# Kernel tuning notes

Measured on AMD Instinct MI355X. Metric: run time of the kernel, lower is better.

## Reference

```python
import math
import jax, jax.numpy as jnp
import numpy as np

B = 16; ENC_S = 64; ENC_T = 96
SCALE = 64; POOL = 16; DM = 256; NH = 16
E_LAYERS = 3; D_LAYERS = 2; DFF = 1024
OUT_S = 64; OUT_T = 32
LN_EPS = 1e-5


def _pe(d_model, length):
    pos = np.arange(length, dtype=np.float32)[:, None]
    div = np.exp(np.arange(0, d_model, 2, dtype=np.float32) * (-math.log(10000.0) / d_model))
    pe = np.zeros((length, d_model), np.float32)
    pe[:, 0::2] = np.sin(pos * div)
    pe[:, 1::2] = np.cos(pos * div)
    return jnp.asarray(pe)


def _conv1d_circ(x, w, b):
    # x: (N, C, L), w: (O, C, 3); torch Conv1d(padding=1, padding_mode='circular')
    xp = jnp.pad(x, ((0, 0), (0, 0), (1, 1)), mode='wrap')
    y = jax.lax.conv_general_dilated(xp, w, (1,), 'VALID',
                                     dimension_numbers=('NCH', 'OIH', 'NCH'))
    return y + b[None, :, None]


def _layernorm(x, w, b):
    mu = jnp.mean(x, -1, keepdims=True)
    var = jnp.var(x, -1, keepdims=True)
    return (x - mu) * jax.lax.rsqrt(var + LN_EPS) * w + b


def _data_embedding(x, sproj_w, sproj_b, scproj_w, scproj_b, tok_w, tok_b):
    Bb = x.shape[0]
    h = _conv1d_circ(jnp.swapaxes(x, 1, 2), sproj_w, sproj_b)       # (B, enc_t, enc_t)
    h = _conv1d_circ(h, scproj_w, scproj_b)                          # (B, scale, enc_t)
    h = _conv1d_circ(jnp.swapaxes(h, 1, 2), scproj_w, scproj_b)     # (B, scale, scale)
    h = h.reshape(Bb * SCALE, 1, SCALE)
    tok = jnp.swapaxes(_conv1d_circ(h, tok_w, tok_b), 1, 2)          # (B*scale, scale, dm)
    emb = tok + _pe(DM, SCALE)[None]
    return emb.reshape(Bb, SCALE, SCALE, DM)


def _lin_attn(q, k, v, causal):
    # q,k,v: (Bp, L, H, E); k/v adaptively avg-pooled over L to POOL (L % POOL == 0)
    Bp, L, H, E = q.shape
    win = L // POOL
    kp = k.reshape(Bp, POOL, win, H, E).mean(axis=2)
    vp = v.reshape(Bp, POOL, win, H, E).mean(axis=2)
    scores = jnp.einsum('blhe,bshe->bhls', q, kp)      # (Bp, H, L, POOL)
    if causal:
        m = jnp.arange(POOL)[None, :] > jnp.arange(L)[:, None]
        scores = jnp.where(m[None, None], -jnp.inf, scores)
    A = jax.nn.softmax(scores / math.sqrt(E), axis=-1)
    return jnp.einsum('bhls,bshd->blhd', A, vp)


def _st_attn(x, kv, Wq, bq, Wo, bo, causal):
    Bb, T, S, dm = x.shape
    H = NH // 2
    proj = lambda z: z @ Wq.T + bq
    # faithful to source: query_projection used for q, k AND v; views are flat reshapes
    qt = proj(x.reshape(Bb * S, T, dm)).reshape(Bb * S, T, H, -1)
    qs = proj(x.reshape(Bb * T, S, dm)).reshape(Bb * T, S, H, -1)
    kt = proj(kv.reshape(Bb * S, T, dm)).reshape(Bb * S, T, H, -1)
    ks = proj(kv.reshape(Bb * T, S, dm)).reshape(Bb * T, S, H, -1)
    out_t = _lin_attn(qt, kt, kt, causal).reshape(Bb, S, T, -1)
    out_s = _lin_attn(qs, ks, ks, causal).reshape(Bb, S, T, -1)
    out = jnp.concatenate([out_t, out_s], axis=-1).reshape(Bb, S * T, 2 * dm)
    out = out @ Wo.T + bo
    return out.reshape(Bb, T, S, dm)


def _ffn(x, c1w, c1b, c2w, c2b):
    # conv1d kernel_size=1 over the T axis of (B*S, T, dm) == pointwise GEMM
    Bb, T, S, dm = x.shape
    y = x.reshape(Bb * S, T, dm)
    y = jax.nn.gelu(jnp.einsum('ntd,fd->ntf', y, c1w) + c1b, approximate=False)
    y = jnp.einsum('ntf,df->ntd', y, c2w) + c2b
    return y.reshape(Bb, T, S, dm)


def _forward(x_enc, x_dec,
             enc_sproj_w, enc_sproj_b, enc_scproj_w, enc_scproj_b, enc_tok_w, enc_tok_b,
             dec_sproj_w, dec_sproj_b, dec_scproj_w, dec_scproj_b, dec_tok_w, dec_tok_b,
             e_Wq, e_bq, e_Wo, e_bo, e_c1w, e_c1b, e_c2w, e_c2b,
             e_ln1w, e_ln1b, e_ln2w, e_ln2b, enc_norm_w, enc_norm_b,
             d_sWq, d_sbq, d_sWo, d_sbo, d_cWq, d_cbq, d_cWo, d_cbo,
             d_c1w, d_c1b, d_c2w, d_c2b,
             d_ln1w, d_ln1b, d_ln2w, d_ln2b, d_ln3w, d_ln3b,
             dec_norm_w, dec_norm_b, proj_w, proj_b):
    enc = _data_embedding(x_enc, enc_sproj_w, enc_sproj_b, enc_scproj_w, enc_scproj_b, enc_tok_w, enc_tok_b)
    for i in range(E_LAYERS):
        h = enc + _st_attn(enc, enc, e_Wq[i], e_bq[i], e_Wo[i], e_bo[i], False)
        h = _layernorm(h, e_ln1w[i], e_ln1b[i])
        enc = _layernorm(h + _ffn(h, e_c1w[i], e_c1b[i], e_c2w[i], e_c2b[i]), e_ln2w[i], e_ln2b[i])
    enc = _layernorm(enc, enc_norm_w, enc_norm_b)
    dec = _data_embedding(x_dec, dec_sproj_w, dec_sproj_b, dec_scproj_w, dec_scproj_b, dec_tok_w, dec_tok_b)
    for i in range(D_LAYERS):
        h = dec + _st_attn(dec, dec, d_sWq[i], d_sbq[i], d_sWo[i], d_sbo[i], True)
        h = _layernorm(h, d_ln1w[i], d_ln1b[i])
        h = h + _st_attn(h, enc, d_cWq[i], d_cbq[i], d_cWo[i], d_cbo[i], False)
        h = _layernorm(h, d_ln2w[i], d_ln2b[i])
        dec = _layernorm(h + _ffn(h, d_c1w[i], d_c1b[i], d_c2w[i], d_c2b[i]), d_ln3w[i], d_ln3b[i])
    dec = _layernorm(dec, dec_norm_w, dec_norm_b)
    dec = dec.mean(axis=2)                 # (B, scale, dm)
    out = dec @ proj_w.T + proj_b          # (B, scale, out_s)
    return out[:, -OUT_T:, :]


def setup_inputs() -> dict:
    keys = iter(jax.random.split(jax.random.key(0), 80))
    def nrm(shape, s=0.02):
        return jax.random.normal(next(keys), shape, jnp.float32) * s
    E, D = E_LAYERS, D_LAYERS
    inp = {
        'x_enc': nrm((B, ENC_T, ENC_S), 1.0),
        'x_dec': nrm((B, ENC_T, ENC_S), 1.0),
    }
    for p in ('enc', 'dec'):
        inp[p + '_sproj_w'] = nrm((ENC_T, ENC_S, 3)); inp[p + '_sproj_b'] = nrm((ENC_T,))
        inp[p + '_scproj_w'] = nrm((SCALE, ENC_T, 3)); inp[p + '_scproj_b'] = nrm((SCALE,))
        inp[p + '_tok_w'] = nrm((DM, 1, 3), 0.1); inp[p + '_tok_b'] = nrm((DM,))
    inp.update(
        e_Wq=nrm((E, DM, DM)), e_bq=nrm((E, DM)),
        e_Wo=nrm((E, DM, 2 * DM)), e_bo=nrm((E, DM)),
        e_c1w=nrm((E, DFF, DM)), e_c1b=nrm((E, DFF)),
        e_c2w=nrm((E, DM, DFF)), e_c2b=nrm((E, DM)),
        e_ln1w=jnp.ones((E, DM)), e_ln1b=jnp.zeros((E, DM)),
        e_ln2w=jnp.ones((E, DM)), e_ln2b=jnp.zeros((E, DM)),
        enc_norm_w=jnp.ones((DM,)), enc_norm_b=jnp.zeros((DM,)),
        d_sWq=nrm((D, DM, DM)), d_sbq=nrm((D, DM)),
        d_sWo=nrm((D, DM, 2 * DM)), d_sbo=nrm((D, DM)),
        d_cWq=nrm((D, DM, DM)), d_cbq=nrm((D, DM)),
        d_cWo=nrm((D, DM, 2 * DM)), d_cbo=nrm((D, DM)),
        d_c1w=nrm((D, DFF, DM)), d_c1b=nrm((D, DFF)),
        d_c2w=nrm((D, DM, DFF)), d_c2b=nrm((D, DM)),
        d_ln1w=jnp.ones((D, DM)), d_ln1b=jnp.zeros((D, DM)),
        d_ln2w=jnp.ones((D, DM)), d_ln2b=jnp.zeros((D, DM)),
        d_ln3w=jnp.ones((D, DM)), d_ln3b=jnp.zeros((D, DM)),
        dec_norm_w=jnp.ones((DM,)), dec_norm_b=jnp.zeros((DM,)),
        proj_w=nrm((OUT_S, DM)), proj_b=nrm((OUT_S,)),
    )
    return inp


def reference(x_enc, x_dec,
              enc_sproj_w, enc_sproj_b, enc_scproj_w, enc_scproj_b, enc_tok_w, enc_tok_b,
              dec_sproj_w, dec_sproj_b, dec_scproj_w, dec_scproj_b, dec_tok_w, dec_tok_b,
              e_Wq, e_bq, e_Wo, e_bo, e_c1w, e_c1b, e_c2w, e_c2b,
              e_ln1w, e_ln1b, e_ln2w, e_ln2b, enc_norm_w, enc_norm_b,
              d_sWq, d_sbq, d_sWo, d_sbo, d_cWq, d_cbq, d_cWo, d_cbo,
              d_c1w, d_c1b, d_c2w, d_c2b,
              d_ln1w, d_ln1b, d_ln2w, d_ln2b, d_ln3w, d_ln3b,
              dec_norm_w, dec_norm_b, proj_w, proj_b):
    return _forward(x_enc, x_dec,
                    enc_sproj_w, enc_sproj_b, enc_scproj_w, enc_scproj_b, enc_tok_w, enc_tok_b,
                    dec_sproj_w, dec_sproj_b, dec_scproj_w, dec_scproj_b, dec_tok_w, dec_tok_b,
                    e_Wq, e_bq, e_Wo, e_bo, e_c1w, e_c1b, e_c2w, e_c2b,
                    e_ln1w, e_ln1b, e_ln2w, e_ln2b, enc_norm_w, enc_norm_b,
                    d_sWq, d_sbq, d_sWo, d_sbo, d_cWq, d_cbq, d_cWo, d_cbo,
                    d_c1w, d_c1b, d_c2w, d_c2b,
                    d_ln1w, d_ln1b, d_ln2w, d_ln2b, d_ln3w, d_ln3b,
                    dec_norm_w, dec_norm_b, proj_w, proj_b)
```

## Files before the change

### kernel.cpp

```cpp
#include <hip/hip_runtime.h>


typedef unsigned short u16;
typedef short s16;
typedef __attribute__((ext_vector_type(8))) s16 bfrag;
typedef __attribute__((ext_vector_type(4))) float f32x4;

__device__ __forceinline__ float b2f(u16 u) {
  union { float f; unsigned int i; } v; v.i = ((unsigned int)u) << 16; return v.f;
}
__device__ __forceinline__ u16 f2b(float f) {
  union { float f; unsigned int i; } v; v.f = f;
  unsigned int x = v.i;
  return (u16)((x + 0x7FFFu + ((x >> 16) & 1u)) >> 16);
}
__device__ __forceinline__ float gelu_f(float v) {
  float u = 0.7978845608f * v * (1.0f + 0.044715f * v * v);
  float e = __expf(2.0f * u);
  return v * (1.0f - 1.0f / (e + 1.0f));
}

__device__ __forceinline__ void gload16(const void* g, void* l) {
  __builtin_amdgcn_global_load_lds(
      (const __attribute__((address_space(1))) unsigned int*)g,
      (__attribute__((address_space(3))) unsigned int*)l, 16, 0, 0);
}

__global__ void ws_signal(float* out, float v) { out[0] = v; }

__global__ void cvt_bf(const float* __restrict__ src, u16* __restrict__ dst, int n) {
  int i = blockIdx.x * 256 + threadIdx.x;
  if (i < n) dst[i] = f2b(src[i]);
}
__global__ void weff_bf(const float* __restrict__ Wo, u16* __restrict__ W) {
  int n = blockIdx.x, k = threadIdx.x;
  W[n * 256 + k] = f2b(Wo[n * 512 + k] + Wo[n * 512 + 256 + k]);
}

__global__ void pe_kernel(float* __restrict__ pe) {
  int l = blockIdx.x, d = threadIdx.x;
  int i = d >> 1;
  float div = expf((float)(2 * i) * (-9.210340371976184f / 256.0f));
  float ang = (float)l * div;
  pe[l * 256 + d] = (d & 1) ? cosf(ang) : sinf(ang);
}

__global__ void conv_sproj(const float* __restrict__ x, const float* __restrict__ w,
                           const float* __restrict__ bias, float* __restrict__ h1) {
  int o = blockIdx.x, b = blockIdx.y, l = threadIdx.x;
  const float* wo = w + o * 192;
  const float* xb = x + (size_t)b * 96 * 64;
  float acc = bias[o];
#pragma unroll
  for (int k = 0; k < 3; ++k) {
    int lp = l + k - 1; if (lp < 0) lp += 96; if (lp >= 96) lp -= 96;
    const float* xr = xb + lp * 64;
    for (int c = 0; c < 64; ++c) acc = fmaf(xr[c], wo[c * 3 + k], acc);
  }
  h1[((size_t)b * 96 + o) * 96 + l] = acc;
}

__global__ void conv_scproj_t(const float* __restrict__ h1, const float* __restrict__ w,
                              const float* __restrict__ bias, float* __restrict__ h2) {
  int o = blockIdx.x, b = blockIdx.y, l = threadIdx.x;
  const float* wo = w + o * 288;
  const float* hb = h1 + (size_t)b * 96 * 96;
  float acc = bias[o];
#pragma unroll
  for (int k = 0; k < 3; ++k) {
    int lp = l + k - 1; if (lp < 0) lp += 96; if (lp >= 96) lp -= 96;
    for (int c = 0; c < 96; ++c) acc = fmaf(hb[c * 96 + lp], wo[c * 3 + k], acc);
  }
  h2[((size_t)b * 64 + o) * 96 + l] = acc;
}

__global__ void conv_scproj_s(const float* __restrict__ h2, const float* __restrict__ w,
                              const float* __restrict__ bias, float* __restrict__ h3) {
  int o = blockIdx.x, b = blockIdx.y, l = threadIdx.x;
  const float* wo = w + o * 288;
  const float* hb = h2 + (size_t)b * 64 * 96;
  float acc = bias[o];
#pragma unroll
  for (int k = 0; k < 3; ++k) {
    int lp = l + k - 1; if (lp < 0) lp += 64; if (lp >= 64) lp -= 64;
    for (int c = 0; c < 96; ++c) acc = fmaf(hb[lp * 96 + c], wo[c * 3 + k], acc);
  }
  h3[((size_t)b * 64 + o) * 64 + l] = acc;
}

__global__ void tok_embed(const float* __restrict__ h3, const float* __restrict__ w,
                          const float* __restrict__ bias, const float* __restrict__ pe,
                          u16* __restrict__ E) {
  int g = blockIdx.x, d = threadIdx.x;
  __shared__ float row[64];
  if (d < 64) row[d] = h3[(size_t)g * 64 + d];
  __syncthreads();
  float w0 = w[d * 3], w1 = w[d * 3 + 1], w2 = w[d * 3 + 2], bd = bias[d];
  for (int j = 0; j < 64; ++j) {
    int jm = (j + 63) & 63, jp = (j + 1) & 63;
    float v = bd + row[jm] * w0 + row[j] * w1 + row[jp] * w2 + pe[j * 256 + d];
    E[((size_t)g * 64 + j) * 256 + d] = f2b(v);
  }
}

template <int ACT, int NBX>
__global__ __launch_bounds__(256) void mfma_gemm(const u16* __restrict__ A,
                                                 const u16* __restrict__ W,
                                                 const float* __restrict__ bias,
                                                 u16* __restrict__ C, int N, int K,
                                                 int nby) {
  __shared__ s16 smem[8192];
  s16* As = smem;
  s16* Bs = smem + 4096;
  constexpr int LB = (NBX == 8) ? 3 : 1;
  int f = blockIdx.x;
  int q = (NBX * nby) >> 3;
  int w = (f & 7) * q + (f >> 3);
  int bx = w & (NBX - 1), by = w >> LB;
  int t = threadIdx.x;
  int wave = t >> 6, lane = t & 63;
  int wr = wave >> 1, wc = wave & 1;
  int row0 = by * 128, col0 = bx * 128;
  int kc = (lane >> 4) & 3, rr = lane & 15;
  const u16* Ap0 = A + (size_t)(row0 + wave * 16 + rr) * K + kc * 8;
  const u16* Ap1 = A + (size_t)(row0 + (wave + 4) * 16 + rr) * K + kc * 8;
  const u16* Bp0 = W + (size_t)(col0 + wave * 16 + rr) * K + kc * 8;
  const u16* Bp1 = W + (size_t)(col0 + (wave + 4) * 16 + rr) * K + kc * 8;
  s16* lA0 = As + wave * 512;
  s16* lA1 = As + (wave + 4) * 512;
  s16* lB0 = Bs + wave * 512;
  s16* lB1 = Bs + (wave + 4) * 512;
  f32x4 acc[4][4];
#pragma unroll
  for (int m = 0; m < 4; ++m)
#pragma unroll
    for (int n = 0; n < 4; ++n) acc[m][n] = (f32x4){0.f, 0.f, 0.f, 0.f};
  for (int k0 = 0; k0 < K; k0 += 32) {
    gload16(Ap0 + k0, lA0);
    gload16(Ap1 + k0, lA1);
    gload16(Bp0 + k0, lB0);
    gload16(Bp1 + k0, lB1);
    __syncthreads();
    bfrag af[4], bf[4];
#pragma unroll
    for (int m = 0; m < 4; ++m) af[m] = *(const bfrag*)(As + ((wr * 4 + m) * 64 + lane) * 8);
#pragma unroll
    for (int n = 0; n < 4; ++n) bf[n] = *(const bfrag*)(Bs + ((wc * 4 + n) * 64 + lane) * 8);
#pragma unroll
    for (int m = 0; m < 4; ++m)
#pragma unroll
      for (int n = 0; n < 4; ++n)
        acc[m][n] = __builtin_amdgcn_mfma_f32_16x16x32_bf16(af[m], bf[n], acc[m][n], 0, 0, 0);
    __syncthreads();
  }
  s16* Cs = smem;
  int g4 = (lane >> 4) << 2;
  int cl = lane & 15;
  float bc[4];
#pragma unroll
  for (int n = 0; n < 4; ++n) bc[n] = bias[col0 + wc * 64 + n * 16 + cl];
#pragma unroll
  for (int P = 0; P < 4; ++P) {
    __syncthreads();
    if (wr == (P >> 1)) {
#pragma unroll
      for (int mm = 0; mm < 2; ++mm) {
        int m = (P & 1) * 2 + mm;
#pragma unroll
        for (int n = 0; n < 4; ++n) {
#pragma unroll
          for (int r = 0; r < 4; ++r) {
            float v = acc[m][n][r] + bc[n];
            if (ACT == 1) v = gelu_f(v);
            Cs[(mm * 16 + g4 + r) * 136 + wc * 64 + n * 16 + cl] = (s16)f2b(v);
          }
        }
      }
    }
    __syncthreads();
#pragma unroll
    for (int it = 0; it < 2; ++it) {
      int idx = it * 256 + t;
      int lr = idx >> 4, slot = idx & 15;
      *(uint4*)(C + (size_t)(row0 + P * 32 + lr) * N + col0 + slot * 8) =
          *(const uint4*)(Cs + lr * 136 + slot * 8);
    }
  }
}

__global__ __launch_bounds__(512) void mfma_gemm_resln(const u16* __restrict__ X,
                                                       const u16* __restrict__ W,
                                                       const float* __restrict__ bias,
                                                       u16* __restrict__ R,
                                                       const float* __restrict__ lnw,
                                                       const float* __restrict__ lnb,
                                                       int K) {
  __shared__ s16 smem[12288];
  __shared__ float pls[32][4][2];
  s16* As = smem;
  s16* Bs = smem + 4096;
  int t = threadIdx.x;
  int wave = t >> 6, lane = t & 63;
  int wr = wave >> 2, wc = wave & 3;
  int row0 = blockIdx.x * 128;
  int kc = (lane >> 4) & 3, rr = lane & 15;
  const u16* Xp = X + (size_t)(row0 + wave * 16 + rr) * K + kc * 8;
  const u16* Wp0 = W + (size_t)(wave * 16 + rr) * K + kc * 8;
  const u16* Wp1 = W + (size_t)((wave + 8) * 16 + rr) * K + kc * 8;
  s16* lA = As + wave * 512;
  s16* lB0 = Bs + wave * 512;
  s16* lB1 = Bs + (wave + 8) * 512;
  f32x4 acc[4][4];
#pragma unroll
  for (int m = 0; m < 4; ++m)
#pragma unroll
    for (int n = 0; n < 4; ++n) acc[m][n] = (f32x4){0.f, 0.f, 0.f, 0.f};
  for (int k0 = 0; k0 < K; k0 += 32) {
    gload16(Xp + k0, lA);
    gload16(Wp0 + k0, lB0);
    gload16(Wp1 + k0, lB1);
    __syncthreads();
    bfrag af[4], bf[4];
#pragma unroll
    for (int m = 0; m < 4; ++m) af[m] = *(const bfrag*)(As + ((wr * 4 + m) * 64 + lane) * 8);
#pragma unroll
    for (int n = 0; n < 4; ++n) bf[n] = *(const bfrag*)(Bs + ((wc * 4 + n) * 64 + lane) * 8);
#pragma unroll
    for (int m = 0; m < 4; ++m)
#pragma unroll
      for (int n = 0; n < 4; ++n)
        acc[m][n] = __builtin_amdgcn_mfma_f32_16x16x32_bf16(af[m], bf[n], acc[m][n], 0, 0, 0);
    __syncthreads();
  }
  s16* Rs = smem;
  int g4 = (lane >> 4) << 2;
  int cl = lane & 15;
  float lw[4], lb[4], bc[4];
#pragma unroll
  for (int n = 0; n < 4; ++n) {
    int col = wc * 64 + n * 16 + cl;
    bc[n] = bias[col]; lw[n] = lnw[col]; lb[n] = lnb[col];
  }
#pragma unroll
  for (int P = 0; P < 4; ++P) {
    bool own = (wr == (P >> 1));
    __syncthreads();
#pragma unroll
    for (int it = 0; it < 2; ++it) {
      int idx = it * 512 + t;
      int lr = idx >> 5, slot = idx & 31;
      *(uint4*)(Rs + lr * 264 + slot * 8) =
          *(const uint4*)(R + (size_t)(row0 + P * 32 + lr) * 256 + slot * 8);
    }
    __syncthreads();
    if (own) {
#pragma unroll
      for (int mm = 0; mm < 2; ++mm) {
        int m = (P & 1) * 2 + mm;
#pragma unroll
        for (int r = 0; r < 4; ++r) {
          int lr = mm * 16 + g4 + r;
          float s = 0.f, s2 = 0.f;
#pragma unroll
          for (int n = 0; n < 4; ++n) {
            float v = acc[m][n][r] + bc[n] +
                      b2f((u16)Rs[lr * 264 + wc * 64 + n * 16 + cl]);
            acc[m][n][r] = v;
            s += v; s2 = fmaf(v, v, s2);
          }
#pragma unroll
          for (int o = 1; o < 16; o <<= 1) { s += __shfl_xor(s, o); s2 += __shfl_xor(s2, o); }
          if (cl == 0) { pls[lr][wc][0] = s; pls[lr][wc][1] = s2; }
        }
      }
    }
    __syncthreads();
    if (own) {
#pragma unroll
      for (int mm = 0; mm < 2; ++mm) {
        int m = (P & 1) * 2 + mm;
#pragma unroll
        for (int r = 0; r < 4; ++r) {
          int lr = mm * 16 + g4 + r;
          float s = pls[lr][0][0] + pls[lr][1][0] + pls[lr][2][0] + pls[lr][3][0];
          float s2 = pls[lr][0][1] + pls[lr][1][1] + pls[lr][2][1] + pls[lr][3][1];
          float mu = s * (1.0f / 256.0f);
          float var = fmaxf(s2 * (1.0f / 256.0f) - mu * mu, 0.0f);
          float rs = rsqrtf(var + 1e-5f);
#pragma unroll
          for (int n = 0; n < 4; ++n) {
            Rs[lr * 264 + wc * 64 + n * 16 + cl] =
                (s16)f2b((acc[m][n][r] - mu) * rs * lw[n] + lb[n]);
          }
        }
      }
    }
    __syncthreads();
#pragma unroll
    for (int it = 0; it < 2; ++it) {
      int idx = it * 512 + t;
      int lr = idx >> 5, slot = idx & 31;
      *(uint4*)(R + (size_t)(row0 + P * 32 + lr) * 256 + slot * 8) =
          *(const uint4*)(Rs + lr * 264 + slot * 8);
    }
  }
}

template <int CROSS, int CAUSAL>
__global__ __launch_bounds__(512) void lin_attn(u16* __restrict__ Q,
                                                const u16* __restrict__ KP) {
  __shared__ u16 qs[64 * 264];
  __shared__ float kpool[16][260];
  int p = blockIdx.x, t = threadIdx.x;
  u16* Qg = Q + (size_t)p * 16384;
#pragma unroll
  for (int i = 0; i < 4; ++i) {
    int idx = i * 512 + t;
    int row = idx >> 5, slot = idx & 31;
    *(uint4*)(qs + row * 264 + slot * 8) = *(const uint4*)(Qg + row * 256 + slot * 8);
  }
  __syncthreads();
  if (CROSS) {
    for (int idx = t; idx < 4096; idx += 512) {
      int s = idx >> 8, d = idx & 255;
      kpool[s][d] = b2f(KP[((size_t)p * 16 + s) * 256 + d]);
    }
  } else {
    for (int idx = t; idx < 4096; idx += 512) {
      int s = idx >> 8, d = idx & 255;
      const u16* b0 = qs + (4 * s) * 264 + d;
      kpool[s][d] = 0.25f * (b2f(b0[0]) + b2f(b0[264]) + b2f(b0[528]) + b2f(b0[792]));
    }
  }
  __syncthreads();
  int h = t >> 6, l = t & 63;
  u16* q = qs + l * 264 + h * 32;
  float qr[32];
#pragma unroll
  for (int e = 0; e < 32; e += 4) {
    ushort4 v = *(const ushort4*)&q[e];
    qr[e] = b2f(v.x); qr[e + 1] = b2f(v.y); qr[e + 2] = b2f(v.z); qr[e + 3] = b2f(v.w);
  }
  float sc[16], mx = -INFINITY;
#pragma unroll
  for (int s = 0; s < 16; ++s) {
    const float* kp = &kpool[s][h * 32];
    float d = 0.f;
#pragma unroll
    for (int e = 0; e < 32; ++e) d = fmaf(qr[e], kp[e], d);
    d *= 0.17677669529663687f;
    if (CAUSAL && s > l) d = -INFINITY;
    sc[s] = d; mx = fmaxf(mx, d);
  }
  float sum = 0.f;
#pragma unroll
  for (int s = 0; s < 16; ++s) { sc[s] = expf(sc[s] - mx); sum += sc[s]; }
  float inv = 1.0f / sum;
  float o[32] = {};
#pragma unroll
  for (int s = 0; s < 16; ++s) {
    float a = sc[s] * inv;
    const float* vp = &kpool[s][h * 32];
#pragma unroll
    for (int e = 0; e < 32; ++e) o[e] = fmaf(a, vp[e], o[e]);
  }
#pragma unroll
  for (int e = 0; e < 32; e += 4) {
    ushort4 v;
    v.x = f2b(o[e]); v.y = f2b(o[e + 1]); v.z = f2b(o[e + 2]); v.w = f2b(o[e + 3]);
    *(ushort4*)&q[e] = v;
  }
  __syncthreads();
#pragma unroll
  for (int i = 0; i < 4; ++i) {
    int idx = i * 512 + t;
    int row = idx >> 5, slot = idx & 31;
    *(uint4*)(Qg + row * 256 + slot * 8) = *(const uint4*)(qs + row * 264 + slot * 8);
  }
}

__global__ __launch_bounds__(256) void ln_bf(u16* __restrict__ X,
                                             const float* __restrict__ w,
                                             const float* __restrict__ b) {
  int lane = threadIdx.x & 63, wv = threadIdx.x >> 6;
  size_t row = (size_t)blockIdx.x * 4 + wv;
  size_t off = row * 256 + lane * 4;
  ushort4 xv = *(const ushort4*)(X + off);
  float v0 = b2f(xv.x), v1 = b2f(xv.y), v2 = b2f(xv.z), v3 = b2f(xv.w);
  float s = v0 + v1 + v2 + v3;
  float s2 = v0 * v0 + v1 * v1 + v2 * v2 + v3 * v3;
#pragma unroll
  for (int o = 32; o; o >>= 1) { s += __shfl_xor(s, o); s2 += __shfl_xor(s2, o); }
  float mu = s * (1.0f / 256.0f);
  float var = fmaxf(s2 * (1.0f / 256.0f) - mu * mu, 0.0f);
  float rs = rsqrtf(var + 1e-5f);
  float4 w4 = *(const float4*)(w + lane * 4);
  float4 b4 = *(const float4*)(b + lane * 4);
  ushort4 o4;
  o4.x = f2b((v0 - mu) * rs * w4.x + b4.x);
  o4.y = f2b((v1 - mu) * rs * w4.y + b4.y);
  o4.z = f2b((v2 - mu) * rs * w4.z + b4.z);
  o4.w = f2b((v3 - mu) * rs * w4.w + b4.w);
  *(ushort4*)(X + off) = o4;
}

__global__ void pool_bf(const u16* __restrict__ A, u16* __restrict__ P) {
  int r = blockIdx.x, d = threadIdx.x;
  int g = r >> 4, s = r & 15;
  const u16* src = A + ((size_t)g * 64 + 4 * (size_t)s) * 256 + d;
  float v = 0.25f * (b2f(src[0]) + b2f(src[256]) + b2f(src[512]) + b2f(src[768]));
  P[(size_t)r * 256 + d] = f2b(v);
}

__global__ __launch_bounds__(256) void mean_proj_bf(const u16* __restrict__ X,
                                                    const float* __restrict__ pw,
                                                    const float* __restrict__ pb,
                                                    float* __restrict__ out) {
  int bid = blockIdx.x;
  int b = bid >> 5, ii = bid & 31;
  int i = 32 + ii;
  __shared__ float md[256];
  int d = threadIdx.x;
  const u16* base = X + ((size_t)b * 64 + i) * 64 * 256 + d;
  float s = 0.f;
  for (int j = 0; j < 64; ++j) s += b2f(base[(size_t)j * 256]);
  md[d] = s * (1.0f / 64.0f);
  __syncthreads();
  if (d < 64) {
    float acc = pb[d];
    const float* wr = pw + d * 256;
    for (int k = 0; k < 256; ++k) acc = fmaf(md[k], wr[k], acc);
    out[((size_t)b * 32 + ii) * 64 + d] = acc;
  }
}

extern "C" void kernel_launch(void* const* d_in, const int* in_sizes, int n_in,
                              void* d_out, int out_size, void* d_ws, size_t ws_size,
                              hipStream_t stream) {
  (void)in_sizes; (void)out_size;
  if (n_in < 50) return;

  const float* x_enc = (const float*)d_in[0];
  const float* x_dec = (const float*)d_in[1];
  const float* enc_sproj_w = (const float*)d_in[2];
  const float* enc_sproj_b = (const float*)d_in[3];
  const float* enc_scproj_w = (const float*)d_in[4];
  const float* enc_scproj_b = (const float*)d_in[5];
  const float* enc_tok_w = (const float*)d_in[6];
  const float* enc_tok_b = (const float*)d_in[7];
  const float* dec_sproj_w = (const float*)d_in[8];
  const float* dec_sproj_b = (const float*)d_in[9];
  const float* dec_scproj_w = (const float*)d_in[10];
  const float* dec_scproj_b = (const float*)d_in[11];
  const float* dec_tok_w = (const float*)d_in[12];
  const float* dec_tok_b = (const float*)d_in[13];
  const float* e_Wq = (const float*)d_in[14];
  const float* e_bq = (const float*)d_in[15];
  const float* e_Wo = (const float*)d_in[16];
  const float* e_bo = (const float*)d_in[17];
  const float* e_c1w = (const float*)d_in[18];
  const float* e_c1b = (const float*)d_in[19];
  const float* e_c2w = (const float*)d_in[20];
  const float* e_c2b = (const float*)d_in[21];
  const float* e_ln1w = (const float*)d_in[22];
  const float* e_ln1b = (const float*)d_in[23];
  const float* e_ln2w = (const float*)d_in[24];
  const float* e_ln2b = (const float*)d_in[25];
  const float* enc_norm_w = (const float*)d_in[26];
  const float* enc_norm_b = (const float*)d_in[27];
  const float* d_sWq = (const float*)d_in[28];
  const float* d_sbq = (const float*)d_in[29];
  const float* d_sWo = (const float*)d_in[30];
  const float* d_sbo = (const float*)d_in[31];
  const float* d_cWq = (const float*)d_in[32];
  const float* d_cbq = (const float*)d_in[33];
  const float* d_cWo = (const float*)d_in[34];
  const float* d_cbo = (const float*)d_in[35];
  const float* d_c1w = (const float*)d_in[36];
  const float* d_c1b = (const float*)d_in[37];
  const float* d_c2w = (const float*)d_in[38];
  const float* d_c2b = (const float*)d_in[39];
  const float* d_ln1w = (const float*)d_in[40];
  const float* d_ln1b = (const float*)d_in[41];
  const float* d_ln2w = (const float*)d_in[42];
  const float* d_ln2b = (const float*)d_in[43];
  const float* d_ln3w = (const float*)d_in[44];
  const float* d_ln3b = (const float*)d_in[45];
  const float* dec_norm_w = (const float*)d_in[46];
  const float* dec_norm_b = (const float*)d_in[47];
  const float* proj_w = (const float*)d_in[48];
  const float* proj_b = (const float*)d_in[49];

  const size_t ACT = 16777216;
  const size_t POOLE = 4194304;
  const size_t WBN = 3538944;
  size_t base_need = (3 * ACT + 2 * POOLE + WBN) * 2 +
                     (size_t)(16384 + 147456 + 98304 + 65536) * 4;
  if (ws_size < base_need) {
    ws_signal<<<1, 1, 0, stream>>>((float*)d_out, (float)(ws_size >> 20));
    return;
  }
  char* wsb = (char*)d_ws;
  u16* A_enc = (u16*)wsb;  wsb += ACT * 2;
  u16* A_dec = (u16*)wsb;  wsb += ACT * 2;
  u16* T1 = (u16*)wsb;     wsb += ACT * 2;
  u16* PA = (u16*)wsb;     wsb += POOLE * 2;
  u16* PK = (u16*)wsb;     wsb += POOLE * 2;
  u16* WB = (u16*)wsb;     wsb += WBN * 2;
  float* PE = (float*)wsb;  wsb += 16384 * 4;
  float* EH1 = (float*)wsb; wsb += 147456 * 4;
  float* EH2 = (float*)wsb; wsb += 98304 * 4;
  float* EH3 = (float*)wsb; wsb += 65536 * 4;

  int hf_rows = 16384;
  u16* HF = T1;
  if (ws_size >= base_need + (size_t)65536 * 1024 * 2) {
    hf_rows = 65536; HF = (u16*)wsb;
  } else if (ws_size >= base_need + (size_t)32768 * 1024 * 2) {
    hf_rows = 32768; HF = (u16*)wsb;
  }

  u16* eWq = WB;
  u16* eWeff = WB + 196608;
  u16* eC1 = WB + 393216;
  u16* eC2 = WB + 1179648;
  u16* dB = WB + 1966080;
  u16* dsWq = dB;
  u16* dsWeff = dB + 131072;
  u16* dcWq = dB + 262144;
  u16* dcWeff = dB + 393216;
  u16* dC1 = dB + 524288;
  u16* dC2 = dB + 1048576;

  cvt_bf<<<768, 256, 0, stream>>>(e_Wq, eWq, 196608);
  cvt_bf<<<3072, 256, 0, stream>>>(e_c1w, eC1, 786432);
  cvt_bf<<<3072, 256, 0, stream>>>(e_c2w, eC2, 786432);
  cvt_bf<<<512, 256, 0, stream>>>(d_sWq, dsWq, 131072);
  cvt_bf<<<512, 256, 0, stream>>>(d_cWq, dcWq, 131072);
  cvt_bf<<<2048, 256, 0, stream>>>(d_c1w, dC1, 524288);
  cvt_bf<<<2048, 256, 0, stream>>>(d_c2w, dC2, 524288);
  for (int i = 0; i < 3; ++i)
    weff_bf<<<256, 256, 0, stream>>>(e_Wo + (size_t)i * 131072, eWeff + (size_t)i * 65536);
  for (int i = 0; i < 2; ++i) {
    weff_bf<<<256, 256, 0, stream>>>(d_sWo + (size_t)i * 131072, dsWeff + (size_t)i * 65536);
    weff_bf<<<256, 256, 0, stream>>>(d_cWo + (size_t)i * 131072, dcWeff + (size_t)i * 65536);
  }

  pe_kernel<<<64, 256, 0, stream>>>(PE);

  conv_sproj<<<dim3(96, 16), 96, 0, stream>>>(x_enc, enc_sproj_w, enc_sproj_b, EH1);
  conv_scproj_t<<<dim3(64, 16), 96, 0, stream>>>(EH1, enc_scproj_w, enc_scproj_b, EH2);
  conv_scproj_s<<<dim3(64, 16), 64, 0, stream>>>(EH2, enc_scproj_w, enc_scproj_b, EH3);
  tok_embed<<<1024, 256, 0, stream>>>(EH3, enc_tok_w, enc_tok_b, PE, A_enc);

  for (int i = 0; i < 3; ++i) {
    mfma_gemm<0, 2><<<1024, 256, 0, stream>>>(A_enc, eWq + (size_t)i * 65536,
                                              e_bq + i * 256, T1, 256, 256, 512);
    lin_attn<0, 0><<<1024, 512, 0, stream>>>(T1, nullptr);
    mfma_gemm_resln<<<512, 512, 0, stream>>>(T1, eWeff + (size_t)i * 65536, e_bo + i * 256,
                                             A_enc, e_ln1w + i * 256, e_ln1b + i * 256, 256);
    for (int m0 = 0; m0 < 65536; m0 += hf_rows) {
      u16* Xc = A_enc + (size_t)m0 * 256;
      int nby = hf_rows / 128;
      mfma_gemm<1, 8><<<8 * nby, 256, 0, stream>>>(
          Xc, eC1 + (size_t)i * 262144, e_c1b + i * 1024, HF, 1024, 256, nby);
      mfma_gemm_resln<<<nby, 512, 0, stream>>>(
          HF, eC2 + (size_t)i * 262144, e_c2b + i * 256, Xc,
          e_ln2w + i * 256, e_ln2b + i * 256, 1024);
    }
  }
  ln_bf<<<16384, 256, 0, stream>>>(A_enc, enc_norm_w, enc_norm_b);
  pool_bf<<<16384, 256, 0, stream>>>(A_enc, PA);

  conv_sproj<<<dim3(96, 16), 96, 0, stream>>>(x_dec, dec_sproj_w, dec_sproj_b, EH1);
  conv_scproj_t<<<dim3(64, 16), 96, 0, stream>>>(EH1, dec_scproj_w, dec_scproj_b, EH2);
  conv_scproj_s<<<dim3(64, 16), 64, 0, stream>>>(EH2, dec_scproj_w, dec_scproj_b, EH3);
  tok_embed<<<1024, 256, 0, stream>>>(EH3, dec_tok_w, dec_tok_b, PE, A_dec);

  for (int i = 0; i < 2; ++i) {
    mfma_gemm<0, 2><<<1024, 256, 0, stream>>>(A_dec, dsWq + (size_t)i * 65536,
                                              d_sbq + i * 256, T1, 256, 256, 512);
    lin_attn<0, 1><<<1024, 512, 0, stream>>>(T1, nullptr);
    mfma_gemm_resln<<<512, 512, 0, stream>>>(T1, dsWeff + (size_t)i * 65536, d_sbo + i * 256,
                                             A_dec, d_ln1w + i * 256, d_ln1b + i * 256, 256);
    mfma_gemm<0, 2><<<1024, 256, 0, stream>>>(A_dec, dcWq + (size_t)i * 65536,
                                              d_cbq + i * 256, T1, 256, 256, 512);
    mfma_gemm<0, 2><<<256, 256, 0, stream>>>(PA, dcWq + (size_t)i * 65536,
                                             d_cbq + i * 256, PK, 256, 256, 128);
    lin_attn<1, 0><<<1024, 512, 0, stream>>>(T1, PK);
    mfma_gemm_resln<<<512, 512, 0, stream>>>(T1, dcWeff + (size_t)i * 65536, d_cbo + i * 256,
                                             A_dec, d_ln2w + i * 256, d_ln2b + i * 256, 256);
    for (int m0 = 0; m0 < 65536; m0 += hf_rows) {
      u16* Xc = A_dec + (size_t)m0 * 256;
      int nby = hf_rows / 128;
      mfma_gemm<1, 8><<<8 * nby, 256, 0, stream>>>(
          Xc, dC1 + (size_t)i * 262144, d_c1b + i * 1024, HF, 1024, 256, nby);
      mfma_gemm_resln<<<nby, 512, 0, stream>>>(
          HF, dC2 + (size_t)i * 262144, d_c2b + i * 256, Xc,
          d_ln3w + i * 256, d_ln3b + i * 256, 1024);
    }
  }
  ln_bf<<<16384, 256, 0, stream>>>(A_dec, dec_norm_w, dec_norm_b);

  mean_proj_bf<<<512, 256, 0, stream>>>(A_dec, proj_w, proj_b, (float*)d_out);
}
```

Before: 1.874 ms.

## Double-buffer LDS tiles in MFMA GEMM kernels to overlap loads with compute

Both the plain and the residual-LayerNorm MFMA GEMM kernels now keep two LDS buffers for the A and B tiles. The global-to-LDS load for the next K step is issued before the MFMAs on the current buffer, which hides load latency and halves the number of barriers per K step. This doubles shared memory per block, which may lower occupancy, especially for the 512-thread resln kernel.

After: 1.898 ms. Within noise of the previous version (+1.3%).

```diff
diff --git a/kernel.cpp b/kernel.cpp
--- a/kernel.cpp
+++ b/kernel.cpp
@@ -109,9 +109,9 @@
                                                  const float* __restrict__ bias,
                                                  u16* __restrict__ C, int N, int K,
                                                  int nby) {
-  __shared__ s16 smem[8192];
-  s16* As = smem;
-  s16* Bs = smem + 4096;
+  __shared__ s16 smem[16384];
+  s16* Asb[2] = {smem, smem + 4096};
+  s16* Bsb[2] = {smem + 8192, smem + 12288};
   constexpr int LB = (NBX == 8) ? 3 : 1;
   int f = blockIdx.x;
   int q = (NBX * nby) >> 3;
@@ -126,32 +126,44 @@
   const u16* Ap1 = A + (size_t)(row0 + (wave + 4) * 16 + rr) * K + kc * 8;
   const u16* Bp0 = W + (size_t)(col0 + wave * 16 + rr) * K + kc * 8;
   const u16* Bp1 = W + (size_t)(col0 + (wave + 4) * 16 + rr) * K + kc * 8;
-  s16* lA0 = As + wave * 512;
-  s16* lA1 = As + (wave + 4) * 512;
-  s16* lB0 = Bs + wave * 512;
-  s16* lB1 = Bs + (wave + 4) * 512;
   f32x4 acc[4][4];
 #pragma unroll
   for (int m = 0; m < 4; ++m)
 #pragma unroll
     for (int n = 0; n < 4; ++n) acc[m][n] = (f32x4){0.f, 0.f, 0.f, 0.f};
-  for (int k0 = 0; k0 < K; k0 += 32) {
-    gload16(Ap0 + k0, lA0);
-    gload16(Ap1 + k0, lA1);
-    gload16(Bp0 + k0, lB0);
-    gload16(Bp1 + k0, lB1);
-    __syncthreads();
+
+  auto STAGE = [&](s16* a, s16* b, int kidx) {
+    int k0 = kidx * 32;
+    gload16(Ap0 + k0, a + wave * 512);
+    gload16(Ap1 + k0, a + (wave + 4) * 512);
+    gload16(Bp0 + k0, b + wave * 512);
+    gload16(Bp1 + k0, b + (wave + 4) * 512);
+  };
+  auto COMPUTE = [&](const s16* a, const s16* b) {
     bfrag af[4], bf[4];
 #pragma unroll
-    for (int m = 0; m < 4; ++m) af[m] = *(const bfrag*)(As + ((wr * 4 + m) * 64 + lane) * 8);
-#pragma unroll
-    for (int n = 0; n < 4; ++n) bf[n] = *(const bfrag*)(Bs + ((wc * 4 + n) * 64 + lane) * 8);
+    for (int m = 0; m < 4; ++m) af[m] = *(const bfrag*)(a + ((wr * 4 + m) * 64 + lane) * 8);
+#pragma unroll
+    for (int n = 0; n < 4; ++n) bf[n] = *(const bfrag*)(b + ((wc * 4 + n) * 64 + lane) * 8);
 #pragma unroll
     for (int m = 0; m < 4; ++m)
 #pragma unroll
       for (int n = 0; n < 4; ++n)
         acc[m][n] = __builtin_amdgcn_mfma_f32_16x16x32_bf16(af[m], bf[n], acc[m][n], 0, 0, 0);
-    __syncthreads();
+  };
+
+  int nk = K >> 5;
+  STAGE(Asb[0], Bsb[0], 0);
+  __syncthreads();
+  for (int ks = 0; ks < nk; ks += 2) {
+    if (ks + 1 < nk) STAGE(Asb[1], Bsb[1], ks + 1);
+    COMPUTE(Asb[0], Bsb[0]);
+    __syncthreads();
+    if (ks + 1 < nk) {
+      if (ks + 2 < nk) STAGE(Asb[0], Bsb[0], ks + 2);
+      COMPUTE(Asb[1], Bsb[1]);
+      __syncthreads();
+    }
   }
   s16* Cs = smem;
   int g4 = (lane >> 4) << 2;
@@ -195,10 +207,10 @@
                                                        const float* __restrict__ lnw,
                                                        const float* __restrict__ lnb,
                                                        int K) {
-  __shared__ s16 smem[12288];
+  __shared__ s16 smem[24576];
   __shared__ float pls[32][4][2];
-  s16* As = smem;
-  s16* Bs = smem + 4096;
+  s16* Asb[2] = {smem, smem + 4096};
+  s16* Bsb[2] = {smem + 8192, smem + 16384};
   int t = threadIdx.x;
   int wave = t >> 6, lane = t & 63;
   int wr = wave >> 2, wc = wave & 3;
@@ -207,30 +219,43 @@
   const u16* Xp = X + (size_t)(row0 + wave * 16 + rr) * K + kc * 8;
   const u16* Wp0 = W + (size_t)(wave * 16 + rr) * K + kc * 8;
   const u16* Wp1 = W + (size_t)((wave + 8) * 16 + rr) * K + kc * 8;
-  s16* lA = As + wave * 512;
-  s16* lB0 = Bs + wave * 512;
-  s16* lB1 = Bs + (wave + 8) * 512;
   f32x4 acc[4][4];
 #pragma unroll
   for (int m = 0; m < 4; ++m)
 #pragma unroll
     for (int n = 0; n < 4; ++n) acc[m][n] = (f32x4){0.f, 0.f, 0.f, 0.f};
-  for (int k0 = 0; k0 < K; k0 += 32) {
-    gload16(Xp + k0, lA);
-    gload16(Wp0 + k0, lB0);
-    gload16(Wp1 + k0, lB1);
-    __syncthreads();
+
+  auto STAGE = [&](s16* a, s16* b, int kidx) {
+    int k0 = kidx * 32;
+    gload16(Xp + k0, a + wave * 512);
+    gload16(Wp0 + k0, b + wave * 512);
+    gload16(Wp1 + k0, b + (wave + 8) * 512);
+  };
+  auto COMPUTE = [&](const s16* a, const s16* b) {
     bfrag af[4], bf[4];
 #pragma unroll
-    for (int m = 0; m < 4; ++m) af[m] = *(const bfrag*)(As + ((wr * 4 + m) * 64 + lane) * 8);
-#pragma unroll
-    for (int n = 0; n < 4; ++n) bf[n] = *(const bfrag*)(Bs + ((wc * 4 + n) * 64 + lane) * 8);
+    for (int m = 0; m < 4; ++m) af[m] = *(const bfrag*)(a + ((wr * 4 + m) * 64 + lane) * 8);
+#pragma unroll
+    for (int n = 0; n < 4; ++n) bf[n] = *(const bfrag*)(b + ((wc * 4 + n) * 64 + lane) * 8);
 #pragma unroll
     for (int m = 0; m < 4; ++m)
 #pragma unroll
       for (int n = 0; n < 4; ++n)
         acc[m][n] = __builtin_amdgcn_mfma_f32_16x16x32_bf16(af[m], bf[n], acc[m][n], 0, 0, 0);
-    __syncthreads();
+  };
+
+  int nk = K >> 5;
+  STAGE(Asb[0], Bsb[0], 0);
+  __syncthreads();
+  for (int ks = 0; ks < nk; ks += 2) {
+    if (ks + 1 < nk) STAGE(Asb[1], Bsb[1], ks + 1);
+    COMPUTE(Asb[0], Bsb[0]);
+    __syncthreads();
+    if (ks + 1 < nk) {
+      if (ks + 2 < nk) STAGE(Asb[0], Bsb[0], ks + 2);
+      COMPUTE(Asb[1], Bsb[1]);
+      __syncthreads();
+    }
   }
   s16* Rs = smem;
   int g4 = (lane >> 4) << 2;
```

## Fuse FFN up-projection, GELU, down-projection and residual LayerNorm into one kernel

Applied to the files above, without the earlier changes.

Replaces the two-kernel FFN (conv1 GEMM writing a 1024-wide hidden activation to global memory, then conv2 GEMM with residual LayerNorm) with a single kernel per 64-row tile. Each tile keeps the activation block in LDS, computes the hidden layer in 128-column chunks, applies GELU into an LDS buffer, and accumulates the down-projection in registers. This removes the global write and re-read of the large hidden tensor and the workspace-size-dependent chunking. In exchange it uses about 112KB of LDS per block, which limits occupancy, and reloads the weight chunks for every 64-row tile without double buffering.

New measurement: 2.070 ms. 1.1x slower.

```diff
diff --git a/kernel.cpp b/kernel.cpp
--- a/kernel.cpp
+++ b/kernel.cpp
@@ -126,20 +126,16 @@
   const u16* Ap1 = A + (size_t)(row0 + (wave + 4) * 16 + rr) * K + kc * 8;
   const u16* Bp0 = W + (size_t)(col0 + wave * 16 + rr) * K + kc * 8;
   const u16* Bp1 = W + (size_t)(col0 + (wave + 4) * 16 + rr) * K + kc * 8;
-  s16* lA0 = As + wave * 512;
-  s16* lA1 = As + (wave + 4) * 512;
-  s16* lB0 = Bs + wave * 512;
-  s16* lB1 = Bs + (wave + 4) * 512;
   f32x4 acc[4][4];
 #pragma unroll
   for (int m = 0; m < 4; ++m)
 #pragma unroll
     for (int n = 0; n < 4; ++n) acc[m][n] = (f32x4){0.f, 0.f, 0.f, 0.f};
   for (int k0 = 0; k0 < K; k0 += 32) {
-    gload16(Ap0 + k0, lA0);
-    gload16(Ap1 + k0, lA1);
-    gload16(Bp0 + k0, lB0);
-    gload16(Bp1 + k0, lB1);
+    gload16(Ap0 + k0, As + wave * 512);
+    gload16(Ap1 + k0, As + (wave + 4) * 512);
+    gload16(Bp0 + k0, Bs + wave * 512);
+    gload16(Bp1 + k0, Bs + (wave + 4) * 512);
     __syncthreads();
     bfrag af[4], bf[4];
 #pragma unroll
@@ -207,18 +203,15 @@
   const u16* Xp = X + (size_t)(row0 + wave * 16 + rr) * K + kc * 8;
   const u16* Wp0 = W + (size_t)(wave * 16 + rr) * K + kc * 8;
   const u16* Wp1 = W + (size_t)((wave + 8) * 16 + rr) * K + kc * 8;
-  s16* lA = As + wave * 512;
-  s16* lB0 = Bs + wave * 512;
-  s16* lB1 = Bs + (wave + 8) * 512;
   f32x4 acc[4][4];
 #pragma unroll
   for (int m = 0; m < 4; ++m)
 #pragma unroll
     for (int n = 0; n < 4; ++n) acc[m][n] = (f32x4){0.f, 0.f, 0.f, 0.f};
   for (int k0 = 0; k0 < K; k0 += 32) {
-    gload16(Xp + k0, lA);
-    gload16(Wp0 + k0, lB0);
-    gload16(Wp1 + k0, lB1);
+    gload16(Xp + k0, As + wave * 512);
+    gload16(Wp0 + k0, Bs + wave * 512);
+    gload16(Wp1 + k0, Bs + (wave + 8) * 512);
     __syncthreads();
     bfrag af[4], bf[4];
 #pragma unroll
@@ -303,6 +296,161 @@
       *(uint4*)(R + (size_t)(row0 + P * 32 + lr) * 256 + slot * 8) =
           *(const uint4*)(Rs + lr * 264 + slot * 8);
     }
+  }
+}
+
+__global__ __launch_bounds__(512) void ffn_fused(u16* __restrict__ A,
+                                                 const u16* __restrict__ C1,
+                                                 const float* __restrict__ b1,
+                                                 const u16* __restrict__ C2,
+                                                 const float* __restrict__ b2,
+                                                 const float* __restrict__ lnw,
+                                                 const float* __restrict__ lnb) {
+  __shared__ s16 XF[16384];
+  __shared__ s16 BF[32768];
+  __shared__ s16 HF[8192];
+  __shared__ float pls[64][4][2];
+  int t = threadIdx.x;
+  int wave = t >> 6, lane = t & 63;
+  int wr = wave >> 2, wc = wave & 3;
+  int row0 = blockIdx.x * 64;
+  int rr = lane & 15, kc = lane >> 4;
+  int g4 = (lane >> 4) << 2, cl = lane & 15;
+
+#pragma unroll
+  for (int i = 0; i < 4; ++i) {
+    int f = wave * 4 + i;
+    int ks = f >> 2, m = f & 3;
+    gload16(A + (size_t)(row0 + m * 16 + rr) * 256 + ks * 32 + kc * 8, XF + f * 512);
+  }
+
+  f32x4 acc2[2][4];
+#pragma unroll
+  for (int mi = 0; mi < 2; ++mi)
+#pragma unroll
+    for (int nj = 0; nj < 4; ++nj) acc2[mi][nj] = (f32x4){0.f, 0.f, 0.f, 0.f};
+
+  for (int hc = 0; hc < 8; ++hc) {
+#pragma unroll
+    for (int i = 0; i < 8; ++i) {
+      int f = i * 8 + wave;
+      int ks = f >> 3, n = f & 7;
+      gload16(C1 + (size_t)(hc * 128 + n * 16 + rr) * 256 + ks * 32 + kc * 8,
+              BF + f * 512);
+    }
+    __syncthreads();
+    f32x4 acc1[2][2];
+#pragma unroll
+    for (int mi = 0; mi < 2; ++mi)
+#pragma unroll
+      for (int ni = 0; ni < 2; ++ni) acc1[mi][ni] = (f32x4){0.f, 0.f, 0.f, 0.f};
+#pragma unroll
+    for (int ks = 0; ks < 8; ++ks) {
+      bfrag a0 = *(const bfrag*)(XF + ((ks * 4 + wr * 2 + 0) * 64 + lane) * 8);
+      bfrag a1 = *(const bfrag*)(XF + ((ks * 4 + wr * 2 + 1) * 64 + lane) * 8);
+      bfrag b0 = *(const bfrag*)(BF + ((ks * 8 + wc * 2 + 0) * 64 + lane) * 8);
+      bfrag b1f = *(const bfrag*)(BF + ((ks * 8 + wc * 2 + 1) * 64 + lane) * 8);
+      acc1[0][0] = __builtin_amdgcn_mfma_f32_16x16x32_bf16(a0, b0, acc1[0][0], 0, 0, 0);
+      acc1[0][1] = __builtin_amdgcn_mfma_f32_16x16x32_bf16(a0, b1f, acc1[0][1], 0, 0, 0);
+      acc1[1][0] = __builtin_amdgcn_mfma_f32_16x16x32_bf16(a1, b0, acc1[1][0], 0, 0, 0);
+      acc1[1][1] = __builtin_amdgcn_mfma_f32_16x16x32_bf16(a1, b1f, acc1[1][1], 0, 0, 0);
+    }
+#pragma unroll
+    for (int ni = 0; ni < 2; ++ni) {
+      float bcol = b1[hc * 128 + wc * 32 + ni * 16 + cl];
+      int kc2 = ni * 2 + (cl >> 3);
+      int e = cl & 7;
+#pragma unroll
+      for (int mi = 0; mi < 2; ++mi) {
+        int fbase = (wc * 4 + wr * 2 + mi) * 512;
+#pragma unroll
+        for (int r = 0; r < 4; ++r) {
+          float v = gelu_f(acc1[mi][ni][r] + bcol);
+          HF[fbase + (g4 + r + kc2 * 16) * 8 + e] = (s16)f2b(v);
+        }
+      }
+    }
+    __syncthreads();
+#pragma unroll
+    for (int i = 0; i < 8; ++i) {
+      int f = i * 8 + wave;
+      int ks2 = f >> 4, n2 = f & 15;
+      gload16(C2 + (size_t)(n2 * 16 + rr) * 1024 + hc * 128 + ks2 * 32 + kc * 8,
+              BF + f * 512);
+    }
+    __syncthreads();
+#pragma unroll
+    for (int ks2 = 0; ks2 < 4; ++ks2) {
+      bfrag a0 = *(const bfrag*)(HF + ((ks2 * 4 + wr * 2 + 0) * 64 + lane) * 8);
+      bfrag a1 = *(const bfrag*)(HF + ((ks2 * 4 + wr * 2 + 1) * 64 + lane) * 8);
+#pragma unroll
+      for (int nj = 0; nj < 4; ++nj) {
+        bfrag bb = *(const bfrag*)(BF + ((ks2 * 16 + wc * 4 + nj) * 64 + lane) * 8);
+        acc2[0][nj] = __builtin_amdgcn_mfma_f32_16x16x32_bf16(a0, bb, acc2[0][nj], 0, 0, 0);
+        acc2[1][nj] = __builtin_amdgcn_mfma_f32_16x16x32_bf16(a1, bb, acc2[1][nj], 0, 0, 0);
+      }
+    }
+    __syncthreads();
+  }
+
+  s16* Rs = BF;
+#pragma unroll
+  for (int it = 0; it < 4; ++it) {
+    int idx = it * 512 + t;
+    int lr = idx >> 5, slot = idx & 31;
+    *(uint4*)(Rs + lr * 264 + slot * 8) =
+        *(const uint4*)(A + (size_t)(row0 + lr) * 256 + slot * 8);
+  }
+  __syncthreads();
+  float lw[4], lb[4], bc2[4];
+#pragma unroll
+  for (int nj = 0; nj < 4; ++nj) {
+    int col = wc * 64 + nj * 16 + cl;
+    bc2[nj] = b2[col]; lw[nj] = lnw[col]; lb[nj] = lnb[col];
+  }
+#pragma unroll
+  for (int mi = 0; mi < 2; ++mi) {
+#pragma unroll
+    for (int r = 0; r < 4; ++r) {
+      int row = wr * 32 + mi * 16 + g4 + r;
+      float s = 0.f, s2 = 0.f;
+#pragma unroll
+      for (int nj = 0; nj < 4; ++nj) {
+        int col = wc * 64 + nj * 16 + cl;
+        float v = acc2[mi][nj][r] + bc2[nj] + b2f((u16)Rs[row * 264 + col]);
+        acc2[mi][nj][r] = v;
+        s += v; s2 = fmaf(v, v, s2);
+      }
+#pragma unroll
+      for (int o = 1; o < 16; o <<= 1) { s += __shfl_xor(s, o); s2 += __shfl_xor(s2, o); }
+      if (cl == 0) { pls[row][wc][0] = s; pls[row][wc][1] = s2; }
+    }
+  }
+  __syncthreads();
+#pragma unroll
+  for (int mi = 0; mi < 2; ++mi) {
+#pragma unroll
+    for (int r = 0; r < 4; ++r) {
+      int row = wr * 32 + mi * 16 + g4 + r;
+      float s = pls[row][0][0] + pls[row][1][0] + pls[row][2][0] + pls[row][3][0];
+      float s2 = pls[row][0][1] + pls[row][1][1] + pls[row][2][1] + pls[row][3][1];
+      float mu = s * (1.0f / 256.0f);
+      float var = fmaxf(s2 * (1.0f / 256.0f) - mu * mu, 0.0f);
+      float rs = rsqrtf(var + 1e-5f);
+#pragma unroll
+      for (int nj = 0; nj < 4; ++nj) {
+        int col = wc * 64 + nj * 16 + cl;
+        Rs[row * 264 + col] = (s16)f2b((acc2[mi][nj][r] - mu) * rs * lw[nj] + lb[nj]);
+      }
+    }
+  }
+  __syncthreads();
+#pragma unroll
+  for (int it = 0; it < 4; ++it) {
+    int idx = it * 512 + t;
+    int lr = idx >> 5, slot = idx & 31;
+    *(uint4*)(A + (size_t)(row0 + lr) * 256 + slot * 8) =
+        *(const uint4*)(Rs + lr * 264 + slot * 8);
   }
 }
 
@@ -512,14 +660,6 @@
   float* EH2 = (float*)wsb; wsb += 98304 * 4;
   float* EH3 = (float*)wsb; wsb += 65536 * 4;
 
-  int hf_rows = 16384;
-  u16* HF = T1;
-  if (ws_size >= base_need + (size_t)65536 * 1024 * 2) {
-    hf_rows = 65536; HF = (u16*)wsb;
-  } else if (ws_size >= base_need + (size_t)32768 * 1024 * 2) {
-    hf_rows = 32768; HF = (u16*)wsb;
-  }
-
   u16* eWq = WB;
   u16* eWeff = WB + 196608;
   u16* eC1 = WB + 393216;
@@ -559,15 +699,9 @@
     lin_attn<0, 0><<<1024, 512, 0, stream>>>(T1, nullptr);
     mfma_gemm_resln<<<512, 512, 0, stream>>>(T1, eWeff + (size_t)i * 65536, e_bo + i * 256,
                                              A_enc, e_ln1w + i * 256, e_ln1b + i * 256, 256);
-    for (int m0 = 0; m0 < 65536; m0 += hf_rows) {
-      u16* Xc = A_enc + (size_t)m0 * 256;
-      int nby = hf_rows / 128;
-      mfma_gemm<1, 8><<<8 * nby, 256, 0, stream>>>(
-          Xc, eC1 + (size_t)i * 262144, e_c1b + i * 1024, HF, 1024, 256, nby);
-      mfma_gemm_resln<<<nby, 512, 0, stream>>>(
-          HF, eC2 + (size_t)i * 262144, e_c2b + i * 256, Xc,
-          e_ln2w + i * 256, e_ln2b + i * 256, 1024);
-    }
+    ffn_fused<<<1024, 512, 0, stream>>>(A_enc, eC1 + (size_t)i * 262144, e_c1b + i * 1024,
+                                        eC2 + (size_t)i * 262144, e_c2b + i * 256,
+                                        e_ln2w + i * 256, e_ln2b + i * 256);
   }
   ln_bf<<<16384, 256, 0, stream>>>(A_enc, enc_norm_w, enc_norm_b);
   pool_bf<<<16384, 256, 0, stream>>>(A_enc, PA);
@@ -590,15 +724,9 @@
     lin_attn<1, 0><<<1024, 512, 0, stream>>>(T1, PK);
     mfma_gemm_resln<<<512, 512, 0, stream>>>(T1, dcWeff + (size_t)i * 65536, d_cbo + i * 256,
                                              A_dec, d_ln2w + i * 256, d_ln2b + i * 256, 256);
-    for (int m0 = 0; m0 < 65536; m0 += hf_rows) {
-      u16* Xc = A_dec + (size_t)m0 * 256;
-      int nby = hf_rows / 128;
-      mfma_gemm<1, 8><<<8 * nby, 256, 0, stream>>>(
-          Xc, dC1 + (size_t)i * 262144, d_c1b + i * 1024, HF, 1024, 256, nby);
-      mfma_gemm_resln<<<nby, 512, 0, stream>>>(
-          HF, dC2 + (size_t)i * 262144, d_c2b + i * 256, Xc,
-          d_ln3w + i * 256, d_ln3b + i * 256, 1024);
-    }
+    ffn_fused<<<1024, 512, 0, stream>>>(A_dec, dC1 + (size_t)i * 262144, d_c1b + i * 1024,
+                                        dC2 + (size_t)i * 262144, d_c2b + i * 256,
+                                        d_ln3w + i * 256, d_ln3b + i * 256);
   }
   ln_bf<<<16384, 256, 0, stream>>>(A_dec, dec_norm_w, dec_norm_b);
 
```

## Load MFMA operands directly from global memory instead of staging through LDS

Applied to the files above, without the earlier changes.

Both GEMM kernels stop staging A/W tiles in shared memory via global_load_lds with two barriers per K step. Each wave now loads its own bf16 fragments straight from global into registers and runs the MFMA loop with no synchronisation, unrolled by two. This removes the barrier stalls and LDS traffic and shrinks shared memory to the epilogue buffer, which can raise occupancy. In exchange, operands shared between waves are fetched redundantly from global/L2, and the per-lane 16-byte loads are strided by K, so coalescing is worse.

Result: slower. 2.475 ms (+32.1%).

```diff
diff --git a/kernel.cpp b/kernel.cpp
--- a/kernel.cpp
+++ b/kernel.cpp
@@ -18,12 +18,6 @@
   float u = 0.7978845608f * v * (1.0f + 0.044715f * v * v);
   float e = __expf(2.0f * u);
   return v * (1.0f - 1.0f / (e + 1.0f));
-}
-
-__device__ __forceinline__ void gload16(const void* g, void* l) {
-  __builtin_amdgcn_global_load_lds(
-      (const __attribute__((address_space(1))) unsigned int*)g,
-      (__attribute__((address_space(3))) unsigned int*)l, 16, 0, 0);
 }
 
 __global__ void ws_signal(float* out, float v) { out[0] = v; }
@@ -109,9 +103,7 @@
                                                  const float* __restrict__ bias,
                                                  u16* __restrict__ C, int N, int K,
                                                  int nby) {
-  __shared__ s16 smem[8192];
-  s16* As = smem;
-  s16* Bs = smem + 4096;
+  __shared__ s16 Cs[4352];
   constexpr int LB = (NBX == 8) ? 3 : 1;
   int f = blockIdx.x;
   int q = (NBX * nby) >> 3;
@@ -120,45 +112,35 @@
   int t = threadIdx.x;
   int wave = t >> 6, lane = t & 63;
   int wr = wave >> 1, wc = wave & 1;
-  int row0 = by * 128, col0 = bx * 128;
-  int kc = (lane >> 4) & 3, rr = lane & 15;
-  const u16* Ap0 = A + (size_t)(row0 + wave * 16 + rr) * K + kc * 8;
-  const u16* Ap1 = A + (size_t)(row0 + (wave + 4) * 16 + rr) * K + kc * 8;
-  const u16* Bp0 = W + (size_t)(col0 + wave * 16 + rr) * K + kc * 8;
-  const u16* Bp1 = W + (size_t)(col0 + (wave + 4) * 16 + rr) * K + kc * 8;
-  s16* lA0 = As + wave * 512;
-  s16* lA1 = As + (wave + 4) * 512;
-  s16* lB0 = Bs + wave * 512;
-  s16* lB1 = Bs + (wave + 4) * 512;
+  int brow = by * 128, bcol = bx * 128;
+  int rr = lane & 15, kb = (lane >> 4) * 8;
+  const u16* Ap = A + (size_t)(brow + wr * 64 + rr) * K + kb;
+  const u16* Wp = W + (size_t)(bcol + wc * 64 + rr) * K + kb;
   f32x4 acc[4][4];
 #pragma unroll
   for (int m = 0; m < 4; ++m)
 #pragma unroll
     for (int n = 0; n < 4; ++n) acc[m][n] = (f32x4){0.f, 0.f, 0.f, 0.f};
-  for (int k0 = 0; k0 < K; k0 += 32) {
-    gload16(Ap0 + k0, lA0);
-    gload16(Ap1 + k0, lA1);
-    gload16(Bp0 + k0, lB0);
-    gload16(Bp1 + k0, lB1);
-    __syncthreads();
-    bfrag af[4], bf[4];
-#pragma unroll
-    for (int m = 0; m < 4; ++m) af[m] = *(const bfrag*)(As + ((wr * 4 + m) * 64 + lane) * 8);
-#pragma unroll
-    for (int n = 0; n < 4; ++n) bf[n] = *(const bfrag*)(Bs + ((wc * 4 + n) * 64 + lane) * 8);
+
+  int nk = K >> 5;
+#pragma unroll 2
+  for (int ks = 0; ks < nk; ++ks) {
+    bfrag a[4], b[4];
+#pragma unroll
+    for (int m = 0; m < 4; ++m) a[m] = *(const bfrag*)(Ap + (size_t)m * 16 * K + ks * 32);
+#pragma unroll
+    for (int n = 0; n < 4; ++n) b[n] = *(const bfrag*)(Wp + (size_t)n * 16 * K + ks * 32);
 #pragma unroll
     for (int m = 0; m < 4; ++m)
 #pragma unroll
       for (int n = 0; n < 4; ++n)
-        acc[m][n] = __builtin_amdgcn_mfma_f32_16x16x32_bf16(af[m], bf[n], acc[m][n], 0, 0, 0);
-    __syncthreads();
-  }
-  s16* Cs = smem;
+        acc[m][n] = __builtin_amdgcn_mfma_f32_16x16x32_bf16(a[m], b[n], acc[m][n], 0, 0, 0);
+  }
   int g4 = (lane >> 4) << 2;
   int cl = lane & 15;
   float bc[4];
 #pragma unroll
-  for (int n = 0; n < 4; ++n) bc[n] = bias[col0 + wc * 64 + n * 16 + cl];
+  for (int n = 0; n < 4; ++n) bc[n] = bias[bcol + wc * 64 + n * 16 + cl];
 #pragma unroll
   for (int P = 0; P < 4; ++P) {
     __syncthreads();
@@ -182,7 +164,7 @@
     for (int it = 0; it < 2; ++it) {
       int idx = it * 256 + t;
       int lr = idx >> 4, slot = idx & 15;
-      *(uint4*)(C + (size_t)(row0 + P * 32 + lr) * N + col0 + slot * 8) =
+      *(uint4*)(C + (size_t)(brow + P * 32 + lr) * N + bcol + slot * 8) =
           *(const uint4*)(Cs + lr * 136 + slot * 8);
     }
   }
@@ -195,44 +177,35 @@
                                                        const float* __restrict__ lnw,
                                                        const float* __restrict__ lnb,
                                                        int K) {
-  __shared__ s16 smem[12288];
+  __shared__ s16 Rs[8448];
   __shared__ float pls[32][4][2];
-  s16* As = smem;
-  s16* Bs = smem + 4096;
   int t = threadIdx.x;
   int wave = t >> 6, lane = t & 63;
   int wr = wave >> 2, wc = wave & 3;
   int row0 = blockIdx.x * 128;
-  int kc = (lane >> 4) & 3, rr = lane & 15;
-  const u16* Xp = X + (size_t)(row0 + wave * 16 + rr) * K + kc * 8;
-  const u16* Wp0 = W + (size_t)(wave * 16 + rr) * K + kc * 8;
-  const u16* Wp1 = W + (size_t)((wave + 8) * 16 + rr) * K + kc * 8;
-  s16* lA = As + wave * 512;
-  s16* lB0 = Bs + wave * 512;
-  s16* lB1 = Bs + (wave + 8) * 512;
+  int rr = lane & 15, kb = (lane >> 4) * 8;
+  const u16* Xp = X + (size_t)(row0 + wr * 64 + rr) * K + kb;
+  const u16* Wp = W + (size_t)(wc * 64 + rr) * K + kb;
   f32x4 acc[4][4];
 #pragma unroll
   for (int m = 0; m < 4; ++m)
 #pragma unroll
     for (int n = 0; n < 4; ++n) acc[m][n] = (f32x4){0.f, 0.f, 0.f, 0.f};
-  for (int k0 = 0; k0 < K; k0 += 32) {
-    gload16(Xp + k0, lA);
-    gload16(Wp0 + k0, lB0);
-    gload16(Wp1 + k0, lB1);
-    __syncthreads();
-    bfrag af[4], bf[4];
-#pragma unroll
-    for (int m = 0; m < 4; ++m) af[m] = *(const bfrag*)(As + ((wr * 4 + m) * 64 + lane) * 8);
-#pragma unroll
-    for (int n = 0; n < 4; ++n) bf[n] = *(const bfrag*)(Bs + ((wc * 4 + n) * 64 + lane) * 8);
+
+  int nk = K >> 5;
+#pragma unroll 2
+  for (int ks = 0; ks < nk; ++ks) {
+    bfrag a[4], b[4];
+#pragma unroll
+    for (int m = 0; m < 4; ++m) a[m] = *(const bfrag*)(Xp + (size_t)m * 16 * K + ks * 32);
+#pragma unroll
+    for (int n = 0; n < 4; ++n) b[n] = *(const bfrag*)(Wp + (size_t)n * 16 * K + ks * 32);
 #pragma unroll
     for (int m = 0; m < 4; ++m)
 #pragma unroll
       for (int n = 0; n < 4; ++n)
-        acc[m][n] = __builtin_amdgcn_mfma_f32_16x16x32_bf16(af[m], bf[n], acc[m][n], 0, 0, 0);
-    __syncthreads();
-  }
-  s16* Rs = smem;
+        acc[m][n] = __builtin_amdgcn_mfma_f32_16x16x32_bf16(a[m], b[n], acc[m][n], 0, 0, 0);
+  }
   int g4 = (lane >> 4) << 2;
   int cl = lane & 15;
   float lw[4], lb[4], bc[4];
```
